# Kernel tuning notes

Measured on AMD Instinct MI355X. Metric: run time of the kernel, lower is better.

## Reference

```python
import jax, jax.numpy as jnp
import numpy as np
import math

B, S, H = 4, 1024, 1024
NH, DH = 16, 64  # MULTI_HEAD, HIDDEN_SIZE_HEAD


def setup_inputs() -> dict:
    key = jax.random.key(0)
    ks = jax.random.split(key, 14)
    w = lambda k: (jax.random.normal(k, (H, H), dtype=jnp.float32) * 0.02)
    b = lambda k: (jax.random.normal(k, (H,), dtype=jnp.float32) * 0.02)
    return {
        "v": jax.random.normal(ks[0], (B, S, H), dtype=jnp.float32),
        "k": jax.random.normal(ks[1], (B, S, H), dtype=jnp.float32),
        "q": jax.random.normal(ks[2], (B, S, H), dtype=jnp.float32),
        "mask": jax.random.randint(ks[3], (B, 1, 1, S), 0, 2) == 1,
        "group_prob": jax.random.uniform(ks[4], (B, S, S), dtype=jnp.float32),
        "Wq": w(ks[5]), "bq": b(ks[6]),
        "Wk": w(ks[7]), "bk": b(ks[8]),
        "Wv": w(ks[9]), "bv": b(ks[10]),
        "Wm": w(ks[11]), "bm": b(ks[12]),
    }


def reference(v, k, q, mask, group_prob, Wq, bq, Wk, bk, Wv, bv, Wm, bm):
    nb = q.shape[0]
    inv_sqrt_dk = 1.0 / math.sqrt(DH)

    def proj(x, W, b):
        # torch Linear: x @ W.T + b, then split heads -> [B, NH, S, DH]
        y = jnp.einsum('bsh,oh->bso', x, W) + b
        return y.reshape(nb, -1, NH, DH).transpose(0, 2, 1, 3)

    qh = proj(q, Wq, bq)
    kh = proj(k, Wk, bk)
    vh = proj(v, Wv, bv)

    scores = jnp.einsum('bhqd,bhkd->bhqk', qh, kh) * inv_sqrt_dk
    scores = jnp.where(mask, jnp.float32(-1e9), scores)
    att = jax.nn.softmax(scores, axis=-1)
    # post-softmax group-prior scaling (the non-standard part)
    att = att * group_prob[:, None, :, :]
    # dropout in eval mode = identity
    out = jnp.einsum('bhqk,bhkd->bhqd', att, vh)
    out = out.transpose(0, 2, 1, 3).reshape(nb, -1, H)
    return jnp.einsum('bsh,oh->bso', out, Wm) + bm
```

## Files before the change

kernel.cpp:

```cpp
#include <hip/hip_runtime.h>

#define S_LEN 1024
#define NHEAD 16
#define DHEAD 64

typedef _Float16 half8 __attribute__((ext_vector_type(8)));
typedef _Float16 half4v __attribute__((ext_vector_type(4)));
typedef float floatx4 __attribute__((ext_vector_type(4)));

#define QSCALE 0.125f
#define EXPSHIFT 4.0f

__device__ __forceinline__ void gll16(const _Float16* g, _Float16* s) {
    __builtin_amdgcn_global_load_lds(
        (const __attribute__((address_space(1))) void*)g,
        (__attribute__((address_space(3))) void*)s, 16, 0, 0);
}

struct SplitArgs {
    const float* src[7];
    _Float16* hi[7];
    int nblk[7];
};

__global__ __launch_bounds__(256) void split_all_kernel(SplitArgs a)
{
    int blk = blockIdx.x, seg = 0, off = 0;
    while (blk >= off + a.nblk[seg]) { off += a.nblk[seg]; ++seg; }
    const int i = (blk - off) * 1024 + threadIdx.x * 4;
    float4 v = *(const float4*)&a.src[seg][i];
    half4v h;
    h.x = (_Float16)v.x; h.y = (_Float16)v.y;
    h.z = (_Float16)v.z; h.w = (_Float16)v.w;
    *(half4v*)&a.hi[seg][i] = h;
}

__global__ __launch_bounds__(256) void gp_prep_kernel(
    const float* __restrict__ gp, _Float16* __restrict__ gpt)
{
    __shared__ _Float16 G[128 * 64];
    const int t = threadIdx.x;
    const int tile = blockIdx.x;
    const int kt = tile & 15, qt = (tile >> 4) & 7, b = tile >> 7;
    const float* src = gp + ((size_t)(b * S_LEN + qt * 128)) * S_LEN + kt * 64;

#pragma unroll
    for (int it = 0; it < 8; ++it) {
        const int idx = it * 256 + t;
        const int q = idx >> 4, kk = (idx & 15) * 4;
        float4 v = *(const float4*)&src[(size_t)q * S_LEN + kk];
        half4v h;
        h.x = (_Float16)v.x; h.y = (_Float16)v.y;
        h.z = (_Float16)v.z; h.w = (_Float16)v.w;
        *(half4v*)&G[q * 64 + kk] = h;
    }
    __syncthreads();

    _Float16* dst = gpt + (size_t)tile * 8192;
#pragma unroll
    for (int ph = 0; ph < 4; ++ph) {
        const int chunk = ph * 256 + t;
        const int l = chunk & 63;
        const int rest = chunk >> 6;
        const int h2 = rest & 1, mt = (rest >> 1) & 1, w = rest >> 2;
        const int qb = w * 32 + mt * 16 + (l >> 4) * 4;
        const int kb = l & 15;
        half8 o;
#pragma unroll
        for (int jj = 0; jj < 2; ++jj)
#pragma unroll
            for (int rg = 0; rg < 4; ++rg)
                o[jj * 4 + rg] = G[(qb + rg) * 64 + kb + (h2 * 2 + jj) * 16];
        *(half8*)&dst[chunk * 8] = o;
    }
}

struct ProjArgs {
    const _Float16* A[3];
    const _Float16* B[3];
    const float* bias[3];
    _Float16* C[3];
};

__global__ __launch_bounds__(256, 3) void proj_gemm_kernel(ProjArgs p)
{
    __shared__ __align__(16) _Float16 Ab[128 * 64];
    __shared__ __align__(16) _Float16 Bb[128 * 64];

    const int bid = blockIdx.x;
    const int xcd = bid & 7;
    const int slot = bid >> 3;
    const int mg = slot & 3;
    const int bx = (slot >> 2) & 7;
    const int z  = slot >> 5;
    const int by = xcd + mg * 8;

    const _Float16* A = p.A[z];
    const _Float16* B = p.B[z];
    const float* bias = p.bias[z];
    _Float16* C = p.C[z];

    const int t = threadIdx.x;
    const int w = t >> 6;
    const int l = t & 63;
    const int r = l & 15;
    const int quad = l >> 4;
    const int k7 = r & 7;
    const int rr = l >> 3, ii = l & 7;
    const int wm = (w >> 1) * 64, wn = (w & 1) * 64;
    const int m0 = by * 128;
    const int n0 = bx * 128;

    floatx4 acc[4][4];
#pragma unroll
    for (int i = 0; i < 4; ++i)
#pragma unroll
        for (int j = 0; j < 4; ++j) acc[i][j] = (floatx4){0.f, 0.f, 0.f, 0.f};

    const _Float16* ssrc = (w < 2) ? A : B;
    _Float16* sdst = (w < 2) ? Ab : Bb;
    const int srow0 = (w < 2) ? m0 : n0;
    const int w01 = w & 1;

    auto stage = [&](int kt) {
        const int k0 = kt * 64;
#pragma unroll
        for (int c = 0; c < 8; ++c) {
            const int R = w01 * 64 + c * 8 + rr;
            const int j = ii ^ (R & 7);
            gll16(ssrc + (size_t)(srow0 + R) * 1024 + k0 + j * 8,
                  sdst + R * 64 + ii * 8);
        }
    };

    stage(0);
    for (int kt = 0; kt < 16; ++kt) {
        __syncthreads();

        half8 ah[4][2], bh[4][2];
#pragma unroll
        for (int i = 0; i < 4; ++i) {
            const int R = wm + i * 16 + r;
            ah[i][0] = *(const half8*)&Ab[R * 64 + ((quad ^ k7) << 3)];
            ah[i][1] = *(const half8*)&Ab[R * 64 + (((4 | quad) ^ k7) << 3)];
        }
#pragma unroll
        for (int j = 0; j < 4; ++j) {
            const int R = wn + j * 16 + r;
            bh[j][0] = *(const half8*)&Bb[R * 64 + ((quad ^ k7) << 3)];
            bh[j][1] = *(const half8*)&Bb[R * 64 + (((4 | quad) ^ k7) << 3)];
        }
        __syncthreads();

        if (kt + 1 < 16) stage(kt + 1);

#pragma unroll
        for (int c = 0; c < 2; ++c)
#pragma unroll
            for (int i = 0; i < 4; ++i)
#pragma unroll
                for (int j = 0; j < 4; ++j)
                    acc[i][j] = __builtin_amdgcn_mfma_f32_16x16x32_f16(
                        ah[i][c], bh[j][c], acc[i][j], 0, 0, 0);
    }

#pragma unroll
    for (int i = 0; i < 4; ++i)
#pragma unroll
        for (int j = 0; j < 4; ++j) {
            const int n = n0 + wn + j * 16 + r;
            const float bv = bias[n];
#pragma unroll
            for (int reg = 0; reg < 4; ++reg) {
                const int m = m0 + wm + i * 16 + quad * 4 + reg;
                float val = acc[i][j][reg] + bv;
                if (z == 0) val *= QSCALE;
                const int b = m >> 10, s = m & 1023;
                const int h = n >> 6, d = n & 63;
                const size_t idx = (z == 2)
                    ? (((size_t)(b * NHEAD + h)) * DHEAD + d) * S_LEN + s
                    : (((size_t)(b * NHEAD + h)) * S_LEN + s) * DHEAD + d;
                C[idx] = (_Float16)val;
            }
        }
}

__global__ __launch_bounds__(256, 2) void out_gemm_kernel(
    const _Float16* __restrict__ A, const _Float16* __restrict__ B,
    const float* __restrict__ bias, float* __restrict__ C)
{
    __shared__ __align__(16) _Float16 Ab[128 * 64];
    __shared__ __align__(16) _Float16 Bb[64 * 64];

    const int bid = blockIdx.x;
    const int xcd = bid & 7;
    const int slot = bid >> 3;
    const int by = xcd + (slot & 3) * 8;
    const int bx = slot >> 2;

    const int t = threadIdx.x;
    const int w = t >> 6;
    const int l = t & 63;
    const int r = l & 15;
    const int quad = l >> 4;
    const int k7 = r & 7;
    const int rr = l >> 3, ii = l & 7;
    const int m0 = by * 128, n0 = bx * 64;

    floatx4 acc[2][4];
#pragma unroll
    for (int mt = 0; mt < 2; ++mt)
#pragma unroll
        for (int j = 0; j < 4; ++j) acc[mt][j] = (floatx4){0.f, 0.f, 0.f, 0.f};

    auto stage = [&](int kt) {
        const int k0 = kt * 64;
        if (w < 2) {
#pragma unroll
            for (int c = 0; c < 8; ++c) {
                const int R = (w & 1) * 64 + c * 8 + rr;
                const int j = ii ^ (R & 7);
                gll16(A + (size_t)(m0 + R) * 1024 + k0 + j * 8,
                      Ab + R * 64 + ii * 8);
            }
        } else {
#pragma unroll
            for (int c = 0; c < 4; ++c) {
                const int R = (w - 2) * 32 + c * 8 + rr;
                const int j = ii ^ (R & 7);
                gll16(B + (size_t)(n0 + R) * 1024 + k0 + j * 8,
                      Bb + R * 64 + ii * 8);
            }
        }
    };

    stage(0);
    for (int kt = 0; kt < 16; ++kt) {
        __syncthreads();

        half8 ah[2][2], bh[4][2];
#pragma unroll
        for (int mt = 0; mt < 2; ++mt) {
            const int R = w * 32 + mt * 16 + r;
            ah[mt][0] = *(const half8*)&Ab[R * 64 + ((quad ^ k7) << 3)];
            ah[mt][1] = *(const half8*)&Ab[R * 64 + (((4 | quad) ^ k7) << 3)];
        }
#pragma unroll
        for (int j = 0; j < 4; ++j) {
            const int R = j * 16 + r;
            bh[j][0] = *(const half8*)&Bb[R * 64 + ((quad ^ k7) << 3)];
            bh[j][1] = *(const half8*)&Bb[R * 64 + (((4 | quad) ^ k7) << 3)];
        }
        __syncthreads();

        if (kt + 1 < 16) stage(kt + 1);

#pragma unroll
        for (int c = 0; c < 2; ++c)
#pragma unroll
            for (int mt = 0; mt < 2; ++mt)
#pragma unroll
                for (int j = 0; j < 4; ++j)
                    acc[mt][j] = __builtin_amdgcn_mfma_f32_16x16x32_f16(
                        ah[mt][c], bh[j][c], acc[mt][j], 0, 0, 0);
    }

#pragma unroll
    for (int mt = 0; mt < 2; ++mt)
#pragma unroll
        for (int j = 0; j < 4; ++j) {
            const int n = n0 + j * 16 + r;
            const float bv = bias[n];
#pragma unroll
            for (int reg = 0; reg < 4; ++reg) {
                const int m = m0 + w * 32 + mt * 16 + quad * 4 + reg;
                C[(size_t)m * 1024 + n] = acc[mt][j][reg] + bv;
            }
        }
}

__global__ __launch_bounds__(256, 2) void attention_mfma_kernel(
    const _Float16* __restrict__ Qhi, const _Float16* __restrict__ Khi,
    const _Float16* __restrict__ Vthi, const _Float16* __restrict__ gpt,
    const int* __restrict__ mask, _Float16* __restrict__ OutHi)
{
    __shared__ __align__(16) _Float16 KhS[4096];
    __shared__ __align__(16) _Float16 VhS[4096];
    __shared__ __align__(16) _Float16 gpS[8192];
    __shared__ __align__(16) _Float16 PS[8192];

    const int t = threadIdx.x;
    const int w = t >> 6;
    const int l = t & 63;
    const int lr = l & 15;
    const int quad = l >> 4;
    const int rr = l >> 3;
    const int ii = l & 7;

    const int h  = blockIdx.x & 15;
    const int qt = (blockIdx.x >> 4) & 7;
    const int b  = blockIdx.x >> 7;
    const int q0 = qt * 128;
    const size_t hb = (size_t)(b * NHEAD + h) * (S_LEN * DHEAD);
    const _Float16* gptile = gpt + (size_t)((b * 8 + qt) * 16) * 8192;

    half8 qfh[2][2];
#pragma unroll
    for (int mt = 0; mt < 2; ++mt)
#pragma unroll
        for (int c = 0; c < 2; ++c) {
            const size_t off = hb + (size_t)(q0 + w * 32 + mt * 16 + lr) * 64 + c * 32 + quad * 8;
            qfh[mt][c] = *(const half8*)&Qhi[off];
        }

    float lpart[2][4];
    floatx4 Oa[2][4];
#pragma unroll
    for (int mt = 0; mt < 2; ++mt)
#pragma unroll
        for (int rg = 0; rg < 4; ++rg) {
            lpart[mt][rg] = 0.0f;
            Oa[mt][rg] = (floatx4){0.f, 0.f, 0.f, 0.f};
        }

    auto stageK = [&](int kt) {
        const int k0n = kt * 64;
#pragma unroll
        for (int c2 = 0; c2 < 2; ++c2) {
            const int c = w * 2 + c2;
            const int row = c * 8 + rr;
            const int j = ii ^ (row & 7);
            gll16(Khi + hb + (size_t)(k0n + row) * 64 + j * 8, KhS + c * 512 + l * 8);
        }
    };
    auto stageVG = [&](int kt) {
        const int k0n = kt * 64;
#pragma unroll
        for (int c2 = 0; c2 < 6; ++c2) {
            const int i = w * 6 + c2;
            if (i < 8) {
                const int row = i * 8 + rr;
                const int j = ii ^ (row & 7);
                gll16(Vthi + hb + (size_t)row * S_LEN + k0n + j * 8, VhS + i * 512 + l * 8);
            } else {
                const int c = i - 8;
                gll16(gptile + (size_t)kt * 8192 + c * 512 + l * 8, gpS + c * 512 + l * 8);
            }
        }
    };

    stageK(0);
    stageVG(0);
    __syncthreads();

    for (int kt = 0; kt < 16; ++kt) {
        const int k0 = kt * 64;

        int mk[4];
#pragma unroll
        for (int j = 0; j < 4; ++j) mk[j] = mask[b * S_LEN + k0 + j * 16 + lr];

        floatx4 sc[2][4];
#pragma unroll
        for (int mt = 0; mt < 2; ++mt)
#pragma unroll
            for (int j = 0; j < 4; ++j) sc[mt][j] = (floatx4){0.f, 0.f, 0.f, 0.f};

#pragma unroll
        for (int j = 0; j < 4; ++j) {
            const int key = j * 16 + lr;
            const int base = key * 64;
            const int k7a = key & 7;
            const half8 kh0 = *(const half8*)&KhS[base + (quad ^ k7a) * 8];
            const half8 kh1 = *(const half8*)&KhS[base + ((4 + quad) ^ k7a) * 8];
#pragma unroll
            for (int mt = 0; mt < 2; ++mt) {
                floatx4 a = sc[mt][j];
                a = __builtin_amdgcn_mfma_f32_16x16x32_f16(qfh[mt][0], kh0, a, 0, 0, 0);
                a = __builtin_amdgcn_mfma_f32_16x16x32_f16(qfh[mt][1], kh1, a, 0, 0, 0);
                sc[mt][j] = a;
            }
        }

        __syncthreads();
        if (kt + 1 < 16) stageK(kt + 1);

#pragma unroll
        for (int mt = 0; mt < 2; ++mt) {
            const half8 g0 = *(const half8*)&gpS[(((w * 2 + mt) * 2 + 0) * 64 + l) * 8];
            const half8 g1 = *(const half8*)&gpS[(((w * 2 + mt) * 2 + 1) * 64 + l) * 8];
            const int qlb = w * 32 + mt * 16 + quad * 4;
#pragma unroll
            for (int j = 0; j < 4; ++j) {
                const int col = j * 16 + lr;
                const int cc = col >> 3, wi = col & 7;
#pragma unroll
                for (int rg = 0; rg < 4; ++rg) {
                    const float p = mk[j] ? 0.0f : __expf(sc[mt][j][rg] - EXPSHIFT);
                    lpart[mt][rg] += p;
                    const float g = (float)((j < 2) ? g0[(j & 1) * 4 + rg]
                                                    : g1[(j & 1) * 4 + rg]);
                    const int qloc = qlb + rg;
                    PS[qloc * 64 + (cc ^ (qloc & 7)) * 8 + wi] = (_Float16)(p * g);
                }
            }
        }

        half8 pf[2][2];
#pragma unroll
        for (int mt = 0; mt < 2; ++mt) {
            const int qloc = w * 32 + mt * 16 + lr;
            const int q7 = qloc & 7;
            pf[mt][0] = *(const half8*)&PS[qloc * 64 + (quad ^ q7) * 8];
            pf[mt][1] = *(const half8*)&PS[qloc * 64 + ((4 + quad) ^ q7) * 8];
        }
#pragma unroll
        for (int dt = 0; dt < 4; ++dt) {
            const int d = dt * 16 + lr;
            const int base = d * 64, d7 = d & 7;
            const half8 vh0 = *(const half8*)&VhS[base + (quad ^ d7) * 8];
            const half8 vh1 = *(const half8*)&VhS[base + ((4 + quad) ^ d7) * 8];
#pragma unroll
            for (int mt = 0; mt < 2; ++mt) {
                floatx4 a = Oa[mt][dt];
                a = __builtin_amdgcn_mfma_f32_16x16x32_f16(pf[mt][0], vh0, a, 0, 0, 0);
                a = __builtin_amdgcn_mfma_f32_16x16x32_f16(pf[mt][1], vh1, a, 0, 0, 0);
                Oa[mt][dt] = a;
            }
        }

        __syncthreads();
        if (kt + 1 < 16) stageVG(kt + 1);
    }

#pragma unroll
    for (int mt = 0; mt < 2; ++mt)
#pragma unroll
        for (int rg = 0; rg < 4; ++rg) {
#pragma unroll
            for (int off = 1; off < 16; off <<= 1)
                lpart[mt][rg] += __shfl_xor(lpart[mt][rg], off, 64);
        }

#pragma unroll
    for (int mt = 0; mt < 2; ++mt)
#pragma unroll
        for (int rg = 0; rg < 4; ++rg) {
            const int s = q0 + w * 32 + mt * 16 + quad * 4 + rg;
            const float linv = 1.0f / lpart[mt][rg];
#pragma unroll
            for (int dt = 0; dt < 4; ++dt) {
                const float val = Oa[mt][dt][rg] * linv;
                const size_t idx = ((size_t)(b * S_LEN + s)) * 1024 + h * 64 + dt * 16 + lr;
                OutHi[idx] = (_Float16)val;
            }
        }
}

extern "C" void kernel_launch(void* const* d_in, const int* in_sizes, int n_in,
                              void* d_out, int out_size, void* d_ws, size_t ws_size,
                              hipStream_t stream) {
    const float* v    = (const float*)d_in[0];
    const float* k    = (const float*)d_in[1];
    const float* q    = (const float*)d_in[2];
    const int*   mask = (const int*)d_in[3];
    const float* gp   = (const float*)d_in[4];
    const float* Wq   = (const float*)d_in[5];
    const float* bq   = (const float*)d_in[6];
    const float* Wk   = (const float*)d_in[7];
    const float* bk   = (const float*)d_in[8];
    const float* Wv   = (const float*)d_in[9];
    const float* bv   = (const float*)d_in[10];
    const float* Wm   = (const float*)d_in[11];
    const float* bm   = (const float*)d_in[12];
    float* out = (float*)d_out;

    uint8_t* w8 = (uint8_t*)d_ws;
    const size_t MB = 1024 * 1024;
    _Float16* q_h  = (_Float16*)(w8 + 0 * MB);
    _Float16* k_h  = (_Float16*)(w8 + 8 * MB);
    _Float16* v_h  = (_Float16*)(w8 + 16 * MB);
    _Float16* Wq_h = (_Float16*)(w8 + 24 * MB);
    _Float16* Wk_h = (_Float16*)(w8 + 26 * MB);
    _Float16* Wv_h = (_Float16*)(w8 + 28 * MB);
    _Float16* Wm_h = (_Float16*)(w8 + 30 * MB);
    _Float16* Qh   = (_Float16*)(w8 + 32 * MB);
    _Float16* Kh   = (_Float16*)(w8 + 40 * MB);
    _Float16* Vt   = (_Float16*)(w8 + 48 * MB);
    _Float16* gpt  = (_Float16*)(w8 + 56 * MB);
    _Float16* at   = (_Float16*)(w8 + 0 * MB);

    SplitArgs sa;
    sa.src[0] = q;  sa.hi[0] = q_h;  sa.nblk[0] = 4096;
    sa.src[1] = k;  sa.hi[1] = k_h;  sa.nblk[1] = 4096;
    sa.src[2] = v;  sa.hi[2] = v_h;  sa.nblk[2] = 4096;
    sa.src[3] = Wq; sa.hi[3] = Wq_h; sa.nblk[3] = 1024;
    sa.src[4] = Wk; sa.hi[4] = Wk_h; sa.nblk[4] = 1024;
    sa.src[5] = Wv; sa.hi[5] = Wv_h; sa.nblk[5] = 1024;
    sa.src[6] = Wm; sa.hi[6] = Wm_h; sa.nblk[6] = 1024;
    split_all_kernel<<<16384, 256, 0, stream>>>(sa);

    gp_prep_kernel<<<512, 256, 0, stream>>>(gp, gpt);

    ProjArgs pa;
    pa.A[0] = q_h; pa.B[0] = Wq_h; pa.bias[0] = bq; pa.C[0] = Qh;
    pa.A[1] = k_h; pa.B[1] = Wk_h; pa.bias[1] = bk; pa.C[1] = Kh;
    pa.A[2] = v_h; pa.B[2] = Wv_h; pa.bias[2] = bv; pa.C[2] = Vt;
    proj_gemm_kernel<<<768, 256, 0, stream>>>(pa);

    attention_mfma_kernel<<<512, 256, 0, stream>>>(
        Qh, Kh, Vt, gpt, mask, at);

    out_gemm_kernel<<<512, 256, 0, stream>>>(
        at, Wm_h, bm, out);
}
```

Before: 237.7 us.

## Double-buffer K/V tiles in attention, prefetch group prior to registers, batch split conversion

The attention kernel now double-buffers the K and V shared-memory tiles. It issues the next tile's async loads at the start of each iteration, which drops one of the two barriers per iteration. The group-prior tile is loaded straight from global memory into registers one step ahead instead of being staged through shared memory, and the mask row is cached in shared memory once per block. Separately, the fp32-to-fp16 split kernel now handles four vectors per thread with a quarter of the blocks, cutting launch overhead. The double buffers enlarge the LDS footprint and the prefetched registers raise register pressure, which could hurt occupancy under launch_bounds(256,2).

After: 229.5 us. -3.5%, faster.

```diff
diff --git a/kernel.cpp b/kernel.cpp
--- a/kernel.cpp
+++ b/kernel.cpp
@@ -27,12 +27,16 @@
 {
     int blk = blockIdx.x, seg = 0, off = 0;
     while (blk >= off + a.nblk[seg]) { off += a.nblk[seg]; ++seg; }
-    const int i = (blk - off) * 1024 + threadIdx.x * 4;
-    float4 v = *(const float4*)&a.src[seg][i];
-    half4v h;
-    h.x = (_Float16)v.x; h.y = (_Float16)v.y;
-    h.z = (_Float16)v.z; h.w = (_Float16)v.w;
-    *(half4v*)&a.hi[seg][i] = h;
+    const int base = (blk - off) * 4096 + threadIdx.x * 4;
+#pragma unroll
+    for (int u = 0; u < 4; ++u) {
+        const int i = base + u * 1024;
+        float4 v = *(const float4*)&a.src[seg][i];
+        half4v h;
+        h.x = (_Float16)v.x; h.y = (_Float16)v.y;
+        h.z = (_Float16)v.z; h.w = (_Float16)v.w;
+        *(half4v*)&a.hi[seg][i] = h;
+    }
 }
 
 __global__ __launch_bounds__(256) void gp_prep_kernel(
@@ -284,10 +288,10 @@
     const _Float16* __restrict__ Vthi, const _Float16* __restrict__ gpt,
     const int* __restrict__ mask, _Float16* __restrict__ OutHi)
 {
-    __shared__ __align__(16) _Float16 KhS[4096];
-    __shared__ __align__(16) _Float16 VhS[4096];
-    __shared__ __align__(16) _Float16 gpS[8192];
+    __shared__ __align__(16) _Float16 KhS[2][4096];
+    __shared__ __align__(16) _Float16 VhS[2][4096];
     __shared__ __align__(16) _Float16 PS[8192];
+    __shared__ int maskS[1024];
 
     const int t = threadIdx.x;
     const int w = t >> 6;
@@ -304,6 +308,8 @@
     const size_t hb = (size_t)(b * NHEAD + h) * (S_LEN * DHEAD);
     const _Float16* gptile = gpt + (size_t)((b * 8 + qt) * 16) * 8192;
 
+    ((int4*)maskS)[t] = ((const int4*)(mask + (size_t)b * S_LEN))[t];
+
     half8 qfh[2][2];
 #pragma unroll
     for (int mt = 0; mt < 2; ++mt)
@@ -323,42 +329,56 @@
             Oa[mt][rg] = (floatx4){0.f, 0.f, 0.f, 0.f};
         }
 
-    auto stageK = [&](int kt) {
+    auto stageK = [&](int kt, int bf) {
         const int k0n = kt * 64;
 #pragma unroll
         for (int c2 = 0; c2 < 2; ++c2) {
             const int c = w * 2 + c2;
             const int row = c * 8 + rr;
             const int j = ii ^ (row & 7);
-            gll16(Khi + hb + (size_t)(k0n + row) * 64 + j * 8, KhS + c * 512 + l * 8);
+            gll16(Khi + hb + (size_t)(k0n + row) * 64 + j * 8,
+                  &KhS[bf][0] + c * 512 + l * 8);
         }
     };
-    auto stageVG = [&](int kt) {
+    auto stageV = [&](int kt, int bf) {
         const int k0n = kt * 64;
 #pragma unroll
-        for (int c2 = 0; c2 < 6; ++c2) {
-            const int i = w * 6 + c2;
-            if (i < 8) {
-                const int row = i * 8 + rr;
-                const int j = ii ^ (row & 7);
-                gll16(Vthi + hb + (size_t)row * S_LEN + k0n + j * 8, VhS + i * 512 + l * 8);
-            } else {
-                const int c = i - 8;
-                gll16(gptile + (size_t)kt * 8192 + c * 512 + l * 8, gpS + c * 512 + l * 8);
-            }
+        for (int c2 = 0; c2 < 2; ++c2) {
+            const int i = w * 2 + c2;
+            const int row = i * 8 + rr;
+            const int j = ii ^ (row & 7);
+            gll16(Vthi + hb + (size_t)row * S_LEN + k0n + j * 8,
+                  &VhS[bf][0] + i * 512 + l * 8);
         }
     };
-
-    stageK(0);
-    stageVG(0);
+    auto loadG = [&](half8 (&g)[2][2], int kt) {
+#pragma unroll
+        for (int mt = 0; mt < 2; ++mt)
+#pragma unroll
+            for (int h2 = 0; h2 < 2; ++h2)
+                g[mt][h2] = *(const half8*)&gptile[(size_t)kt * 8192 +
+                    (((w * 2 + mt) * 2 + h2) * 64 + l) * 8];
+    };
+
+    half8 gc[2][2], gn[2][2];
+    stageK(0, 0);
+    stageV(0, 0);
+    loadG(gc, 0);
     __syncthreads();
 
     for (int kt = 0; kt < 16; ++kt) {
+        const int bf = kt & 1;
         const int k0 = kt * 64;
 
+        if (kt + 1 < 16) {
+            stageK(kt + 1, bf ^ 1);
+            stageV(kt + 1, bf ^ 1);
+            loadG(gn, kt + 1);
+        }
+
         int mk[4];
 #pragma unroll
-        for (int j = 0; j < 4; ++j) mk[j] = mask[b * S_LEN + k0 + j * 16 + lr];
+        for (int j = 0; j < 4; ++j) mk[j] = maskS[k0 + j * 16 + lr];
 
         floatx4 sc[2][4];
 #pragma unroll
@@ -371,8 +391,8 @@
             const int key = j * 16 + lr;
             const int base = key * 64;
             const int k7a = key & 7;
-            const half8 kh0 = *(const half8*)&KhS[base + (quad ^ k7a) * 8];
-            const half8 kh1 = *(const half8*)&KhS[base + ((4 + quad) ^ k7a) * 8];
+            const half8 kh0 = *(const half8*)&KhS[bf][base + (quad ^ k7a) * 8];
+            const half8 kh1 = *(const half8*)&KhS[bf][base + ((4 + quad) ^ k7a) * 8];
 #pragma unroll
             for (int mt = 0; mt < 2; ++mt) {
                 floatx4 a = sc[mt][j];
@@ -382,13 +402,10 @@
             }
         }
 
-        __syncthreads();
-        if (kt + 1 < 16) stageK(kt + 1);
-
 #pragma unroll
         for (int mt = 0; mt < 2; ++mt) {
-            const half8 g0 = *(const half8*)&gpS[(((w * 2 + mt) * 2 + 0) * 64 + l) * 8];
-            const half8 g1 = *(const half8*)&gpS[(((w * 2 + mt) * 2 + 1) * 64 + l) * 8];
+            const half8 g0 = gc[mt][0];
+            const half8 g1 = gc[mt][1];
             const int qlb = w * 32 + mt * 16 + quad * 4;
 #pragma unroll
             for (int j = 0; j < 4; ++j) {
@@ -418,8 +435,8 @@
         for (int dt = 0; dt < 4; ++dt) {
             const int d = dt * 16 + lr;
             const int base = d * 64, d7 = d & 7;
-            const half8 vh0 = *(const half8*)&VhS[base + (quad ^ d7) * 8];
-            const half8 vh1 = *(const half8*)&VhS[base + ((4 + quad) ^ d7) * 8];
+            const half8 vh0 = *(const half8*)&VhS[bf][base + (quad ^ d7) * 8];
+            const half8 vh1 = *(const half8*)&VhS[bf][base + ((4 + quad) ^ d7) * 8];
 #pragma unroll
             for (int mt = 0; mt < 2; ++mt) {
                 floatx4 a = Oa[mt][dt];
@@ -430,7 +447,13 @@
         }
 
         __syncthreads();
-        if (kt + 1 < 16) stageVG(kt + 1);
+
+        if (kt + 1 < 16) {
+#pragma unroll
+            for (int mt = 0; mt < 2; ++mt)
+#pragma unroll
+                for (int h2 = 0; h2 < 2; ++h2) gc[mt][h2] = gn[mt][h2];
+        }
     }
 
 #pragma unroll
@@ -491,14 +514,14 @@
     _Float16* at   = (_Float16*)(w8 + 0 * MB);
 
     SplitArgs sa;
-    sa.src[0] = q;  sa.hi[0] = q_h;  sa.nblk[0] = 4096;
-    sa.src[1] = k;  sa.hi[1] = k_h;  sa.nblk[1] = 4096;
-    sa.src[2] = v;  sa.hi[2] = v_h;  sa.nblk[2] = 4096;
-    sa.src[3] = Wq; sa.hi[3] = Wq_h; sa.nblk[3] = 1024;
-    sa.src[4] = Wk; sa.hi[4] = Wk_h; sa.nblk[4] = 1024;
-    sa.src[5] = Wv; sa.hi[5] = Wv_h; sa.nblk[5] = 1024;
-    sa.src[6] = Wm; sa.hi[6] = Wm_h; sa.nblk[6] = 1024;
-    split_all_kernel<<<16384, 256, 0, stream>>>(sa);
+    sa.src[0] = q;  sa.hi[0] = q_h;  sa.nblk[0] = 1024;
+    sa.src[1] = k;  sa.hi[1] = k_h;  sa.nblk[1] = 1024;
+    sa.src[2] = v;  sa.hi[2] = v_h;  sa.nblk[2] = 1024;
+    sa.src[3] = Wq; sa.hi[3] = Wq_h; sa.nblk[3] = 256;
+    sa.src[4] = Wk; sa.hi[4] = Wk_h; sa.nblk[4] = 256;
+    sa.src[5] = Wv; sa.hi[5] = Wv_h; sa.nblk[5] = 256;
+    sa.src[6] = Wm; sa.hi[6] = Wm_h; sa.nblk[6] = 256;
+    split_all_kernel<<<4096, 256, 0, stream>>>(sa);
 
     gp_prep_kernel<<<512, 256, 0, stream>>>(gp, gpt);
 
```
